# Kernel optimization log

Hardware: AMD Instinct MI355X
Metric: run time of the kernel (lower is better)

## Reference

```python
import jax, jax.numpy as jnp
import numpy as np

N_EMBD = 1024
N_HEAD = 16
B, T = 8, 1024
EPS = 1e-5


def setup_inputs() -> dict:
    key = jax.random.key(0)
    ks = jax.random.split(key, 12)
    C = N_EMBD
    s_in = 1.0 / np.sqrt(C)
    s_ff = 1.0 / np.sqrt(4 * C)
    inp = {
        "x": jax.random.normal(ks[0], (B, T, C), dtype=jnp.float32),
        "mask": jnp.tril(jnp.ones((T, T), dtype=jnp.int32))[None, None, :, :],
        "ln1_w": jnp.ones((C,), jnp.float32),
        "ln1_b": jnp.zeros((C,), jnp.float32),
        "ln2_w": jnp.ones((C,), jnp.float32),
        "ln2_b": jnp.zeros((C,), jnp.float32),
        "wq": jax.random.normal(ks[1], (C, C), jnp.float32) * s_in,
        "bq": jnp.zeros((C,), jnp.float32),
        "wk": jax.random.normal(ks[2], (C, C), jnp.float32) * s_in,
        "bk": jnp.zeros((C,), jnp.float32),
        "wv": jax.random.normal(ks[3], (C, C), jnp.float32) * s_in,
        "bv": jnp.zeros((C,), jnp.float32),
        "wo": jax.random.normal(ks[4], (C, C), jnp.float32) * s_in,
        "bo": jnp.zeros((C,), jnp.float32),
        "w1": jax.random.normal(ks[5], (C, 4 * C), jnp.float32) * s_in,
        "b1": jnp.zeros((4 * C,), jnp.float32),
        "w2": jax.random.normal(ks[6], (4 * C, C), jnp.float32) * s_ff,
        "b2": jnp.zeros((C,), jnp.float32),
    }
    return inp


def _layer_norm(x, w, b):
    mu = jnp.mean(x, axis=-1, keepdims=True)
    var = jnp.mean(jnp.square(x - mu), axis=-1, keepdims=True)
    return (x - mu) * jax.lax.rsqrt(var + EPS) * w + b


def reference(x, mask, ln1_w, ln1_b, ln2_w, ln2_b,
              wq, bq, wk, bk, wv, bv, wo, bo, w1, b1, w2, b2):
    Bx, Tx, C = x.shape
    H = N_HEAD
    d = C // H
    h = _layer_norm(x, ln1_w, ln1_b)
    q = (h @ wq + bq).reshape(Bx, Tx, H, d)
    k = (h @ wk + bk).reshape(Bx, Tx, H, d)
    v = (h @ wv + bv).reshape(Bx, Tx, H, d)
    # [B,H,Tq,Tk] scores, scaled by sqrt(head_dim)
    scores = jnp.einsum('bqhd,bkhd->bhqk', q, k) / jnp.sqrt(jnp.float32(d))
    scores = jnp.where(mask == 0, -jnp.inf, scores)
    attn = jax.nn.softmax(scores, axis=-1)
    ctx = jnp.einsum('bhqk,bkhd->bqhd', attn, v).reshape(Bx, Tx, C)
    x = x + (ctx @ wo + bo)
    h2 = _layer_norm(x, ln2_w, ln2_b)
    ff = jax.nn.gelu(h2 @ w1 + b1, approximate=False) @ w2 + b2
    return x + ff
```

## Files before the change

### kernel.cpp

```cpp
#include <hip/hip_runtime.h>
#include <hip/hip_bf16.h>
#include <math.h>


#define DEVI __device__ __forceinline__

typedef __attribute__((ext_vector_type(4))) float floatx4;
typedef __attribute__((ext_vector_type(16))) float floatx16;
typedef __attribute__((ext_vector_type(8))) short shortx8;

DEVI ushort f2b(float f) {
    __hip_bfloat16 h = __float2bfloat16(f);
    return __builtin_bit_cast(ushort, h);
}

DEVI void gl_lds16(const ushort* g, ushort* l) {
    __builtin_amdgcn_global_load_lds(
        (const __attribute__((address_space(1))) void*)g,
        (__attribute__((address_space(3))) void*)l, 16, 0, 0);
}

DEVI float gelu_f(float v) {
    const float u0 = 0.7978845608f * v * (1.0f + 0.044715f * v * v);
    const float u  = fminf(fmaxf(u0, -15.0f), 15.0f);
    const float e  = exp2f(u * 2.885390082f);
    const float th = 1.0f - 2.0f / (e + 1.0f);
    return 0.5f * v * (1.0f + th);
}

__global__ void transp4_kernel(const float* __restrict__ s0, const float* __restrict__ s1,
                               const float* __restrict__ s2, const float* __restrict__ s3,
                               ushort* __restrict__ d0, ushort* __restrict__ d1,
                               ushort* __restrict__ d2, ushort* __restrict__ d3) {
    const int z = blockIdx.z;
    const float* src = (z == 0) ? s0 : (z == 1) ? s1 : (z == 2) ? s2 : s3;
    ushort*      dst = (z == 0) ? d0 : (z == 1) ? d1 : (z == 2) ? d2 : d3;
    __shared__ float tile[32][33];
    const int c0 = blockIdx.x * 32, r0 = blockIdx.y * 32;
    const int tx = threadIdx.x, ty = threadIdx.y;
#pragma unroll
    for (int i = 0; i < 32; i += 8)
        tile[ty + i][tx] = src[(size_t)(r0 + ty + i) * 1024 + c0 + tx];
    __syncthreads();
#pragma unroll
    for (int i = 0; i < 32; i += 8)
        dst[(size_t)(c0 + ty + i) * 1024 + r0 + tx] = f2b(tile[tx][ty + i]);
}

__global__ void transp_kernel(const float* __restrict__ src,
                              ushort* __restrict__ dst, int R, int C) {
    __shared__ float tile[32][33];
    const int c0 = blockIdx.x * 32, r0 = blockIdx.y * 32;
    const int tx = threadIdx.x, ty = threadIdx.y;
#pragma unroll
    for (int i = 0; i < 32; i += 8)
        tile[ty + i][tx] = src[(size_t)(r0 + ty + i) * C + c0 + tx];
    __syncthreads();
#pragma unroll
    for (int i = 0; i < 32; i += 8)
        dst[(size_t)(c0 + ty + i) * R + r0 + tx] = f2b(tile[tx][ty + i]);
}

__global__ __launch_bounds__(256)
void ln_kernel(const float* __restrict__ x, const float* __restrict__ w,
               const float* __restrict__ b, ushort* __restrict__ out) {
    __shared__ float red[8];
    const int m = blockIdx.x;
    const int tid = threadIdx.x;
    const float4 xv = *(const float4*)&x[(size_t)m * 1024 + tid * 4];
    float s  = xv.x + xv.y + xv.z + xv.w;
    float s2 = xv.x * xv.x + xv.y * xv.y + xv.z * xv.z + xv.w * xv.w;
#pragma unroll
    for (int o = 32; o >= 1; o >>= 1) {
        s  += __shfl_xor(s, o, 64);
        s2 += __shfl_xor(s2, o, 64);
    }
    const int wv_ = tid >> 6;
    if ((tid & 63) == 0) { red[wv_] = s; red[4 + wv_] = s2; }
    __syncthreads();
    s  = red[0] + red[1] + red[2] + red[3];
    s2 = red[4] + red[5] + red[6] + red[7];
    const float mu   = s * (1.0f / 1024.0f);
    const float var  = s2 * (1.0f / 1024.0f) - mu * mu;
    const float rstd = rsqrtf(var + 1e-5f);
    const float4 wv = *(const float4*)&w[tid * 4];
    const float4 bv = *(const float4*)&b[tid * 4];
    ushort o4[4];
    o4[0] = f2b((xv.x - mu) * rstd * wv.x + bv.x);
    o4[1] = f2b((xv.y - mu) * rstd * wv.y + bv.y);
    o4[2] = f2b((xv.z - mu) * rstd * wv.z + bv.z);
    o4[3] = f2b((xv.w - mu) * rstd * wv.w + bv.w);
    *(uint2*)&out[(size_t)m * 1024 + tid * 4] = *(uint2*)o4;
}

template <int MODE>
__global__ __launch_bounds__(256, 2)
void gemm_big(const ushort* __restrict__ A, const ushort* __restrict__ Bt,
              const float* __restrict__ biasQ, const float* __restrict__ biasK,
              const float* __restrict__ biasV,
              void* __restrict__ out, void* __restrict__ out2, void* __restrict__ out3,
              int N, int K) {
    __shared__ ushort lds[(256 + 128) * 64];
    ushort* sA = lds;
    ushort* sB = lds + 256 * 64;

    const int tid  = threadIdx.x;
    const int lane = tid & 63;
    const int wave = tid >> 6;
    const int l31  = lane & 31;
    const int half = lane >> 5;
    const int wm   = (wave & 1) * 128;
    const int wn   = (wave >> 1) * 64;
    const int m0   = blockIdx.y * 256;
    const int n0   = blockIdx.x * 128;

    floatx16 acc[4][2] = {};

    const int lrow = lane >> 3;
    const int scb  = (lane & 7) ^ lrow;
    const ushort* Ag = A  + (size_t)(m0 + wave * 8 + lrow) * K + scb * 8;
    const ushort* Bg = Bt + (size_t)(n0 + wave * 8 + lrow) * K + scb * 8;

    for (int k0 = 0; k0 < K; k0 += 64) {
        __syncthreads();
#pragma unroll
        for (int p = 0; p < 8; ++p)
            gl_lds16(Ag + (size_t)(p * 32) * K + k0, sA + (p * 32 + wave * 8) * 64);
#pragma unroll
        for (int p = 0; p < 4; ++p)
            gl_lds16(Bg + (size_t)(p * 32) * K + k0, sB + (p * 32 + wave * 8) * 64);
        __syncthreads();
#pragma unroll
        for (int ks = 0; ks < 4; ++ks) {
            const int cx = ks * 2 + half;
            shortx8 af[4], bf[2];
#pragma unroll
            for (int i = 0; i < 4; ++i) {
                const int r = wm + i * 32 + l31;
                af[i] = *(const shortx8*)&sA[r * 64 + (cx ^ (r & 7)) * 8];
            }
#pragma unroll
            for (int j = 0; j < 2; ++j) {
                const int r = wn + j * 32 + l31;
                bf[j] = *(const shortx8*)&sB[r * 64 + (cx ^ (r & 7)) * 8];
            }
#pragma unroll
            for (int i = 0; i < 4; ++i)
#pragma unroll
                for (int j = 0; j < 2; ++j)
                    acc[i][j] = __builtin_amdgcn_mfma_f32_32x32x16_bf16(
                        af[i], bf[j], acc[i][j], 0, 0, 0);
        }
    }

    if constexpr (MODE == 1) {
        const int mat = n0 >> 10;
        if (mat < 2) {
            const float* bp = (mat == 0) ? biasQ : biasK;
            ushort* dst = (mat == 0) ? (ushort*)out : (ushort*)out2;
            const int bb = m0 >> 10;
            const int tbase = m0 & 1023;
#pragma unroll
            for (int i = 0; i < 4; ++i)
#pragma unroll
                for (int j = 0; j < 2; ++j) {
                    const int cn = (n0 & 1023) + wn + j * 32 + l31;
                    const float bv = bp[cn];
                    const int h = cn >> 6, dd = cn & 63;
#pragma unroll
                    for (int reg = 0; reg < 16; ++reg) {
                        const int t = tbase + wm + i * 32 + (reg & 3) + 8 * (reg >> 2) + 4 * half;
                        dst[((size_t)(bb * 16 + h) * 1024 + t) * 64 + dd] =
                            f2b(acc[i][j][reg] + bv);
                    }
                }
        } else {
            ushort* T = lds;
            const int vb = n0 - 2048;
            const int bb = m0 >> 10;
#pragma unroll
            for (int hf = 0; hf < 2; ++hf) {
                __syncthreads();
                if ((wave & 1) == hf) {
#pragma unroll
                    for (int i = 0; i < 4; ++i)
#pragma unroll
                        for (int j = 0; j < 2; ++j) {
                            const int dim = wn + j * 32 + l31;
                            const float bv = biasV[vb + dim];
#pragma unroll
                            for (int rq = 0; rq < 4; ++rq) {
                                const int tloc = i * 32 + 8 * rq + 4 * half;
                                ushort pk[4];
#pragma unroll
                                for (int e = 0; e < 4; ++e)
                                    pk[e] = f2b(acc[i][j][rq * 4 + e] + bv);
                                *(uint2*)&T[dim * 136 + tloc] = *(uint2*)pk;
                            }
                        }
                }
                __syncthreads();
#pragma unroll
                for (int pass = 0; pass < 8; ++pass) {
                    const int row = pass * 16 + (tid >> 4);
                    const int cb  = (tid & 15) * 8;
                    const uint4 val = *(const uint4*)&T[row * 136 + cb];
                    const int dd = vb + row;
                    const int h = dd >> 6, dl = dd & 63;
                    const int t = (m0 & 1023) + hf * 128 + cb;
                    *(uint4*)&((ushort*)out3)[((size_t)(bb * 16 + h) * 64 + dl) * 1024 + t] = val;
                }
            }
        }
    } else {
#pragma unroll
        for (int i = 0; i < 4; ++i)
#pragma unroll
            for (int j = 0; j < 2; ++j) {
                const int gn = n0 + wn + j * 32 + l31;
                const float bv = biasQ[gn];
#pragma unroll
                for (int reg = 0; reg < 16; ++reg) {
                    const int gm = m0 + wm + i * 32 + (reg & 3) + 8 * (reg >> 2) + 4 * half;
                    const float v = acc[i][j][reg] + bv;
                    ((ushort*)out)[(size_t)gm * N + gn] = f2b(gelu_f(v));
                }
            }
    }
}

__global__ __launch_bounds__(256)
void gemm_res(const ushort* __restrict__ A, const ushort* __restrict__ Bt,
              const float* __restrict__ bias, float* __restrict__ out,
              const float* __restrict__ resid, int N, int K) {
    __shared__ ushort lds[128 * 64 * 2];
    ushort* sA = lds;
    ushort* sB = lds + 128 * 64;

    const int tid  = threadIdx.x;
    const int lane = tid & 63;
    const int wave = tid >> 6;
    const int l31  = lane & 31;
    const int half = lane >> 5;
    const int wm   = (wave & 1) * 64;
    const int wn   = (wave >> 1) * 64;
    const int m0   = blockIdx.y * 128;
    const int n0   = blockIdx.x * 128;

    floatx16 acc[2][2] = {};

    const int lrow = lane >> 3;
    const int scb  = (lane & 7) ^ lrow;
    const ushort* Ag = A  + (size_t)(m0 + wave * 8 + lrow) * K + scb * 8;
    const ushort* Bg = Bt + (size_t)(n0 + wave * 8 + lrow) * K + scb * 8;

    for (int k0 = 0; k0 < K; k0 += 64) {
        __syncthreads();
#pragma unroll
        for (int p = 0; p < 4; ++p) {
            gl_lds16(Ag + (size_t)(p * 32) * K + k0, sA + (p * 32 + wave * 8) * 64);
            gl_lds16(Bg + (size_t)(p * 32) * K + k0, sB + (p * 32 + wave * 8) * 64);
        }
        __syncthreads();
#pragma unroll
        for (int ks = 0; ks < 4; ++ks) {
            const int cx = ks * 2 + half;
            shortx8 af[2], bf[2];
#pragma unroll
            for (int i = 0; i < 2; ++i) {
                const int r = wm + i * 32 + l31;
                af[i] = *(const shortx8*)&sA[r * 64 + (cx ^ (r & 7)) * 8];
            }
#pragma unroll
            for (int j = 0; j < 2; ++j) {
                const int r = wn + j * 32 + l31;
                bf[j] = *(const shortx8*)&sB[r * 64 + (cx ^ (r & 7)) * 8];
            }
#pragma unroll
            for (int i = 0; i < 2; ++i)
#pragma unroll
                for (int j = 0; j < 2; ++j)
                    acc[i][j] = __builtin_amdgcn_mfma_f32_32x32x16_bf16(
                        af[i], bf[j], acc[i][j], 0, 0, 0);
        }
    }
#pragma unroll
    for (int i = 0; i < 2; ++i)
#pragma unroll
        for (int j = 0; j < 2; ++j) {
            const int gn = n0 + wn + j * 32 + l31;
            const float bv = bias[gn];
#pragma unroll
            for (int reg = 0; reg < 16; ++reg) {
                const int gm = m0 + wm + i * 32 + (reg & 3) + 8 * (reg >> 2) + 4 * half;
                out[(size_t)gm * N + gn] =
                    acc[i][j][reg] + bv + resid[(size_t)gm * N + gn];
            }
        }
}

__global__ __launch_bounds__(256)
void attn_kernel(const ushort* __restrict__ Q, const ushort* __restrict__ Kk,
                 const ushort* __restrict__ Vt, ushort* __restrict__ ctx) {
    __shared__ ushort sK[64 * 64];
    __shared__ ushort sV[64 * 64];
    __shared__ ushort sP[4][16 * 72];

    const int tid  = threadIdx.x;
    const int lane = tid & 63;
    const int wave = tid >> 6;
    const int quad = lane >> 4;
    const int l15  = lane & 15;

    const int qb = 15 - (blockIdx.x >> 7);
    const int bh = blockIdx.x & 127;
    const size_t base = (size_t)bh << 16;
    const int bb = bh >> 4, h = bh & 15;

    const int lrow = lane >> 3;
    const int scb  = (lane & 7) ^ lrow;
    const ushort* Kg = Kk + base + (size_t)(wave * 8 + lrow) * 64 + scb * 8;
    const ushort* Vg = Vt + base + (size_t)(wave * 8 + lrow) * 1024 + scb * 8;

    const int qrow = qb * 64 + wave * 16 + l15;
    const shortx8 qf0 = *(const shortx8*)&Q[base + (size_t)qrow * 64 + quad * 8];
    const shortx8 qf1 = *(const shortx8*)&Q[base + (size_t)qrow * 64 + 32 + quad * 8];

    const float SC = 0.125f * 1.44269504f;

    float mstate[4], lstate[4];
    floatx4 oacc[4] = {};
#pragma unroll
    for (int r = 0; r < 4; ++r) { mstate[r] = -__builtin_inff(); lstate[r] = 0.0f; }

    for (int kt = 0; kt <= qb; ++kt) {
        __syncthreads();
#pragma unroll
        for (int p = 0; p < 2; ++p) {
            gl_lds16(Kg + (size_t)kt * 4096 + (size_t)p * 2048,
                     sK + (p * 32 + wave * 8) * 64);
            gl_lds16(Vg + (size_t)kt * 64 + (size_t)p * 32 * 1024,
                     sV + (p * 32 + wave * 8) * 64);
        }
        __syncthreads();

        floatx4 s[4];
#pragma unroll
        for (int nt = 0; nt < 4; ++nt) {
            const int r = nt * 16 + l15;
            const int c0 = quad ^ (r & 7);
            const int c1 = (4 + quad) ^ (r & 7);
            const shortx8 kf0 = *(const shortx8*)&sK[r * 64 + c0 * 8];
            const shortx8 kf1 = *(const shortx8*)&sK[r * 64 + c1 * 8];
            floatx4 z = {};
            z = __builtin_amdgcn_mfma_f32_16x16x32_bf16(qf0, kf0, z, 0, 0, 0);
            z = __builtin_amdgcn_mfma_f32_16x16x32_bf16(qf1, kf1, z, 0, 0, 0);
            s[nt] = z;
        }
#pragma unroll
        for (int nt = 0; nt < 4; ++nt)
#pragma unroll
            for (int r = 0; r < 4; ++r) {
                float sv = s[nt][r] * SC;
                if (kt == qb) {
                    const int col = nt * 16 + l15;
                    const int row = wave * 16 + quad * 4 + r;
                    if (col > row) sv = -__builtin_inff();
                }
                s[nt][r] = sv;
            }
        float mnew[4], alpha[4];
#pragma unroll
        for (int r = 0; r < 4; ++r) {
            float mt = fmaxf(fmaxf(s[0][r], s[1][r]), fmaxf(s[2][r], s[3][r]));
#pragma unroll
            for (int o = 8; o >= 1; o >>= 1) mt = fmaxf(mt, __shfl_xor(mt, o, 64));
            mnew[r]  = fmaxf(mstate[r], mt);
            alpha[r] = exp2f(mstate[r] - mnew[r]);
            mstate[r] = mnew[r];
        }
#pragma unroll
        for (int r = 0; r < 4; ++r) {
            float rs = 0.0f;
#pragma unroll
            for (int nt = 0; nt < 4; ++nt) {
                const float p = exp2f(s[nt][r] - mnew[r]);
                s[nt][r] = p;
                rs += p;
            }
#pragma unroll
            for (int o = 8; o >= 1; o >>= 1) rs += __shfl_xor(rs, o, 64);
            lstate[r] = alpha[r] * lstate[r] + rs;
#pragma unroll
            for (int dt = 0; dt < 4; ++dt) oacc[dt][r] *= alpha[r];
        }
#pragma unroll
        for (int nt = 0; nt < 4; ++nt)
#pragma unroll
            for (int r = 0; r < 4; ++r)
                sP[wave][(quad * 4 + r) * 72 + nt * 16 + l15] = f2b(s[nt][r]);
        __asm__ volatile("s_waitcnt lgkmcnt(0)" ::: "memory");
        const shortx8 pf0 = *(const shortx8*)&sP[wave][l15 * 72 + quad * 8];
        const shortx8 pf1 = *(const shortx8*)&sP[wave][l15 * 72 + 32 + quad * 8];
#pragma unroll
        for (int dt = 0; dt < 4; ++dt) {
            const int r = dt * 16 + l15;
            const int c0 = quad ^ (r & 7);
            const int c1 = (4 + quad) ^ (r & 7);
            const shortx8 v0 = *(const shortx8*)&sV[r * 64 + c0 * 8];
            const shortx8 v1 = *(const shortx8*)&sV[r * 64 + c1 * 8];
            oacc[dt] = __builtin_amdgcn_mfma_f32_16x16x32_bf16(pf0, v0, oacc[dt], 0, 0, 0);
            oacc[dt] = __builtin_amdgcn_mfma_f32_16x16x32_bf16(pf1, v1, oacc[dt], 0, 0, 0);
        }
    }
#pragma unroll
    for (int dt = 0; dt < 4; ++dt)
#pragma unroll
        for (int r = 0; r < 4; ++r) {
            const int t = qb * 64 + wave * 16 + quad * 4 + r;
            const int dim = dt * 16 + l15;
            const float v = oacc[dt][r] / lstate[r];
            ctx[(size_t)(bb * 1024 + t) * 1024 + h * 64 + dim] = f2b(v);
        }
}

extern "C" void kernel_launch(void* const* d_in, const int* in_sizes, int n_in,
                              void* d_out, int out_size, void* d_ws, size_t ws_size,
                              hipStream_t stream) {
    const float* x    = (const float*)d_in[0];
    const float* ln1w = (const float*)d_in[2];
    const float* ln1b = (const float*)d_in[3];
    const float* ln2w = (const float*)d_in[4];
    const float* ln2b = (const float*)d_in[5];
    const float* wq   = (const float*)d_in[6];
    const float* bq   = (const float*)d_in[7];
    const float* wk   = (const float*)d_in[8];
    const float* bk   = (const float*)d_in[9];
    const float* wv   = (const float*)d_in[10];
    const float* bv   = (const float*)d_in[11];
    const float* wo   = (const float*)d_in[12];
    const float* bo   = (const float*)d_in[13];
    const float* w1   = (const float*)d_in[14];
    const float* b1   = (const float*)d_in[15];
    const float* w2   = (const float*)d_in[16];
    const float* b2   = (const float*)d_in[17];

    char* ws = (char*)d_ws;
    const size_t MB = 1024 * 1024;
    ushort* WQKVT = (ushort*)(ws + 0 * MB);
    ushort* WOT   = (ushort*)(ws + 6 * MB);
    ushort* W1T   = (ushort*)(ws + 8 * MB);
    ushort* W2T   = (ushort*)(ws + 16 * MB);
    ushort* H1    = (ushort*)(ws + 24 * MB);
    ushort* H2    = H1;
    ushort* Qb    = (ushort*)(ws + 40 * MB);
    ushort* Kb    = (ushort*)(ws + 56 * MB);
    ushort* Vbt   = (ushort*)(ws + 72 * MB);
    ushort* FF1   = (ushort*)(ws + 40 * MB);
    ushort* CTX   = (ushort*)(ws + 104 * MB);

    float* xout = (float*)d_out;

    const dim3 tb(32, 8);
    transp4_kernel<<<dim3(32, 32, 4), tb, 0, stream>>>(
        wq, wk, wv, wo,
        WQKVT, WQKVT + 1024 * 1024, WQKVT + 2048 * 1024, WOT);
    transp_kernel<<<dim3(128, 32), tb, 0, stream>>>(w1, W1T, 1024, 4096);
    transp_kernel<<<dim3(32, 128), tb, 0, stream>>>(w2, W2T, 4096, 1024);

    ln_kernel<<<8192, 256, 0, stream>>>(x, ln1w, ln1b, H1);

    gemm_big<1><<<dim3(24, 32), 256, 0, stream>>>(H1, WQKVT, bq, bk, bv,
                                                  Qb, Kb, Vbt, 3072, 1024);

    attn_kernel<<<2048, 256, 0, stream>>>(Qb, Kb, Vbt, CTX);

    gemm_res<<<dim3(8, 64), 256, 0, stream>>>(CTX, WOT, bo, xout, x, 1024, 1024);

    ln_kernel<<<8192, 256, 0, stream>>>(xout, ln2w, ln2b, H2);

    gemm_big<3><<<dim3(32, 32), 256, 0, stream>>>(H2, W1T, b1, nullptr, nullptr,
                                                  FF1, nullptr, nullptr, 4096, 1024);

    gemm_res<<<dim3(8, 64), 256, 0, stream>>>(FF1, W2T, b2, xout, xout, 1024, 4096);

    (void)in_sizes; (void)n_in; (void)out_size; (void)ws_size;
}
```

Measured before the change: 511.7 us.

## Split-K the residual GEMMs with atomics and remap block IDs for XCD locality

The residual GEMMs now split K in half across twice as many blocks and accumulate into a zeroed output with float atomic adds. The first half adds the bias, and the residual too for the attention projection. The second FFN GEMM accumulates straight onto the existing output, so it no longer reads the residual separately. All GEMMs use a 1D grid whose block index is remapped so that consecutive M tiles land on the same chiplet group, which should improve L2 reuse. This adds a memset and atomic traffic, and makes the fp32 summation order nondeterministic.

```diff
diff --git a/kernel.cpp b/kernel.cpp
--- a/kernel.cpp
+++ b/kernel.cpp
@@ -99,7 +99,7 @@
               const float* __restrict__ biasQ, const float* __restrict__ biasK,
               const float* __restrict__ biasV,
               void* __restrict__ out, void* __restrict__ out2, void* __restrict__ out3,
-              int N, int K) {
+              int N, int K, int NXT) {
     __shared__ ushort lds[(256 + 128) * 64];
     ushort* sA = lds;
     ushort* sB = lds + 256 * 64;
@@ -111,8 +111,14 @@
     const int half = lane >> 5;
     const int wm   = (wave & 1) * 128;
     const int wn   = (wave >> 1) * 64;
-    const int m0   = blockIdx.y * 256;
-    const int n0   = blockIdx.x * 128;
+
+    const int id = blockIdx.x;
+    const int c  = id & 7;
+    const int q  = id >> 3;
+    const int jx = q % NXT;
+    const int gg = q / NXT;
+    const int m0 = (gg * 8 + c) * 256;
+    const int n0 = jx * 128;
 
     floatx16 acc[4][2] = {};
 
@@ -229,6 +235,7 @@
     }
 }
 
+template <int FOLD_RESID>
 __global__ __launch_bounds__(256)
 void gemm_res(const ushort* __restrict__ A, const ushort* __restrict__ Bt,
               const float* __restrict__ bias, float* __restrict__ out,
@@ -244,8 +251,18 @@
     const int half = lane >> 5;
     const int wm   = (wave & 1) * 64;
     const int wn   = (wave >> 1) * 64;
-    const int m0   = blockIdx.y * 128;
-    const int n0   = blockIdx.x * 128;
+
+    const int id = blockIdx.x;
+    const int c  = id & 7;
+    const int q  = id >> 3;
+    const int jx = q & 7;
+    const int g  = q >> 3;
+    const int mk = g * 8 + c;
+    const int m0 = (mk & 63) * 128;
+    const int kh = mk >> 6;
+    const int n0 = jx * 128;
+    const int Kh = K >> 1;
+    const int kend = kh * Kh + Kh;
 
     floatx16 acc[2][2] = {};
 
@@ -254,7 +271,7 @@
     const ushort* Ag = A  + (size_t)(m0 + wave * 8 + lrow) * K + scb * 8;
     const ushort* Bg = Bt + (size_t)(n0 + wave * 8 + lrow) * K + scb * 8;
 
-    for (int k0 = 0; k0 < K; k0 += 64) {
+    for (int k0 = kh * Kh; k0 < kend; k0 += 64) {
         __syncthreads();
 #pragma unroll
         for (int p = 0; p < 4; ++p) {
@@ -284,6 +301,7 @@
                         af[i], bf[j], acc[i][j], 0, 0, 0);
         }
     }
+    const bool lead = (kh == 0);
 #pragma unroll
     for (int i = 0; i < 2; ++i)
 #pragma unroll
@@ -293,10 +311,16 @@
 #pragma unroll
             for (int reg = 0; reg < 16; ++reg) {
                 const int gm = m0 + wm + i * 32 + (reg & 3) + 8 * (reg >> 2) + 4 * half;
-                out[(size_t)gm * N + gn] =
-                    acc[i][j][reg] + bv + resid[(size_t)gm * N + gn];
-            }
-        }
+                float v = acc[i][j][reg];
+                if (lead) {
+                    v += bv;
+                    if constexpr (FOLD_RESID)
+                        v += resid[(size_t)gm * N + gn];
+                }
+                unsafeAtomicAdd(&out[(size_t)gm * N + gn], v);
+            }
+        }
+    (void)resid;
 }
 
 __global__ __launch_bounds__(256)
@@ -461,6 +485,8 @@
 
     float* xout = (float*)d_out;
 
+    hipMemsetAsync(xout, 0, (size_t)8192 * 1024 * sizeof(float), stream);
+
     const dim3 tb(32, 8);
     transp4_kernel<<<dim3(32, 32, 4), tb, 0, stream>>>(
         wq, wk, wv, wo,
@@ -470,19 +496,19 @@
 
     ln_kernel<<<8192, 256, 0, stream>>>(x, ln1w, ln1b, H1);
 
-    gemm_big<1><<<dim3(24, 32), 256, 0, stream>>>(H1, WQKVT, bq, bk, bv,
-                                                  Qb, Kb, Vbt, 3072, 1024);
+    gemm_big<1><<<768, 256, 0, stream>>>(H1, WQKVT, bq, bk, bv,
+                                         Qb, Kb, Vbt, 3072, 1024, 24);
 
     attn_kernel<<<2048, 256, 0, stream>>>(Qb, Kb, Vbt, CTX);
 
-    gemm_res<<<dim3(8, 64), 256, 0, stream>>>(CTX, WOT, bo, xout, x, 1024, 1024);
+    gemm_res<1><<<1024, 256, 0, stream>>>(CTX, WOT, bo, xout, x, 1024, 1024);
 
     ln_kernel<<<8192, 256, 0, stream>>>(xout, ln2w, ln2b, H2);
 
-    gemm_big<3><<<dim3(32, 32), 256, 0, stream>>>(H2, W1T, b1, nullptr, nullptr,
-                                                  FF1, nullptr, nullptr, 4096, 1024);
-
-    gemm_res<<<dim3(8, 64), 256, 0, stream>>>(FF1, W2T, b2, xout, xout, 1024, 4096);
+    gemm_big<3><<<1024, 256, 0, stream>>>(H2, W1T, b1, nullptr, nullptr,
+                                          FF1, nullptr, nullptr, 4096, 1024, 32);
+
+    gemm_res<0><<<1024, 256, 0, stream>>>(FF1, W2T, b2, xout, nullptr, 1024, 4096);
 
     (void)in_sizes; (void)n_in; (void)out_size; (void)ws_size;
 }
```

After: 586.6 us. 1.15x slower.
